# Optimization experiments

Measured on AMD Instinct MI355X. Metric: run time of the kernel, lower is better.

Reference implementation:

```python
import jax, jax.numpy as jnp
import numpy as np

B, S, L, H, N_ITEMS = 16, 20, 64, 768, 50000  # sessions, max items/session, tokens/item, hidden, catalog
T = S * L
TEMP = 0.05       # config.temp
PAD_POS = 50      # pad item position id (see torch code)
EPS = 1e-8        # torch CosineSimilarity eps


def setup_inputs() -> dict:
    key = jax.random.key(0)
    k1, k2, k3, k4 = jax.random.split(key, 4)
    hidden = jax.random.normal(k1, (B, T, H), jnp.float32)
    emb = jax.random.normal(k2, (N_ITEMS, H), jnp.float32)
    # item position ids: each item's L tokens share position 1..S; padded items -> 50
    pos = np.tile(np.repeat(np.arange(1, S + 1), L)[None, :], (B, 1))  # [B,T]
    sess_len = np.asarray(jax.random.randint(k3, (B,), S // 2, S + 1))  # items per session
    item_idx = np.repeat(np.arange(S), L)[None, :]                      # [1,T]
    pos = np.where(item_idx < sess_len[:, None], pos, PAD_POS).astype(np.int32)
    attn = (pos != PAD_POS).astype(np.int32)
    attrs = np.asarray(jax.random.randint(k4, (B, T), 0, 4)).astype(np.int32)
    return {
        "hidden_states": hidden,
        "item_embedding": emb,
        "attention_mask": jnp.asarray(attn),
        "item_position_ids": jnp.asarray(pos),
        "attr_type_ids": jnp.asarray(attrs),
    }


def reference(hidden_states, item_embedding, attention_mask, item_position_ids, attr_type_ids):
    # --- RecformerPooler (pooler_type='item'): nan-mean pool tokens per item ---
    item_ids = jnp.arange(1, S + 1, dtype=item_position_ids.dtype)
    mask = item_position_ids[:, None, :] == item_ids[None, :, None]      # [B,S,T]
    counts = mask.sum(-1)                                                # [B,S]
    valid = counts > 0                                                   # items present in session
    maskf = mask.astype(hidden_states.dtype)
    pooled = jnp.einsum('bst,bth->bsh', maskf, hidden_states)
    pooled = pooled / jnp.maximum(counts, 1)[..., None].astype(hidden_states.dtype)
    # (torch produces NaN rows for invalid items; we carry `valid` instead)

    # --- Similarity: cosine / temp vs full item catalog ---
    pn = jnp.maximum(jnp.linalg.norm(pooled, axis=-1, keepdims=True), EPS)
    en = jnp.maximum(jnp.linalg.norm(item_embedding, axis=-1, keepdims=True), EPS)
    sim = jnp.einsum('bsh,nh->bns', pooled / pn, item_embedding / en) / TEMP  # [B,N,S]

    # --- reduce_session('maxsim'): NaN -> -inf, max over session items ---
    sim = jnp.where(valid[:, None, :], sim, -jnp.inf)
    scores = sim.max(axis=-1)  # [B, N]; trailing mean over attr dim (size 1) is identity
    return scores
```

## Files before the change

kernel.cpp:

```cpp
#include <hip/hip_runtime.h>

#define B_ 16
#define S_ 20
#define L_ 64
#define T_ 1280
#define H_ 768
#define NITEMS 50000
#define TEMP 0.05f
#define EPSN 1e-8f

#define BM 80
#define BN 128
#define BK 32
#define NKT (H_ / BK)

typedef __attribute__((ext_vector_type(8))) short short8;
typedef __attribute__((ext_vector_type(4))) short short4v;
typedef __attribute__((ext_vector_type(4))) float f32x4;

__device__ __forceinline__ unsigned short f2bf(float f) {
    unsigned int u = __float_as_uint(f);
    u = u + 0x7FFFu + ((u >> 16) & 1u);
    return (unsigned short)(u >> 16);
}

__global__ __launch_bounds__(256) void pool_kernel(const float* __restrict__ hidden,
                                                   const int* __restrict__ pos,
                                                   unsigned short* __restrict__ A,
                                                   int* __restrict__ valid) {
    const int row = blockIdx.x;
    const int b = row / S_, s = row % S_;
    const int tid = threadIdx.x;
    const float* hbase = hidden + ((size_t)b * T_ + (size_t)s * L_) * H_;
    const int* pbase = pos + b * T_ + s * L_;

    float sum0 = 0.f, sum1 = 0.f, sum2 = 0.f;
    int cnt = 0;
#pragma unroll 4
    for (int t = 0; t < L_; ++t) {
        if (pbase[t] == s + 1) {
            const float* hp = hbase + (size_t)t * H_;
            sum0 += hp[tid];
            sum1 += hp[tid + 256];
            sum2 += hp[tid + 512];
            ++cnt;
        }
    }
    const float inv = 1.0f / (float)(cnt > 0 ? cnt : 1);
    const float a0 = sum0 * inv, a1 = sum1 * inv, a2 = sum2 * inv;

    float ss = a0 * a0 + a1 * a1 + a2 * a2;
#pragma unroll
    for (int off = 32; off; off >>= 1) ss += __shfl_xor(ss, off, 64);
    __shared__ float red[4];
    const int wave = tid >> 6, lane = tid & 63;
    if (lane == 0) red[wave] = ss;
    __syncthreads();
    const float tot = red[0] + red[1] + red[2] + red[3];
    const float pn = fmaxf(sqrtf(tot), EPSN);
    const float scale = 1.0f / (pn * TEMP);

    unsigned short* outp = A + (size_t)row * H_;
    outp[tid]       = f2bf(a0 * scale);
    outp[tid + 256] = f2bf(a1 * scale);
    outp[tid + 512] = f2bf(a2 * scale);
    if (tid == 0) valid[row] = (cnt > 0) ? 1 : 0;
}

__global__ __launch_bounds__(256) void gemm_kernel(const float* __restrict__ emb,
                                                   const unsigned short* __restrict__ A,
                                                   const int* __restrict__ valid,
                                                   float* __restrict__ out) {
    const int ntile = blockIdx.x;
    const int mtile = blockIdx.y;
    const int n0 = ntile * BN, m0 = mtile * BM;
    const int tid = threadIdx.x;
    const int wave = tid >> 6, lane = tid & 63, quad = lane >> 4, lq = lane & 15;

    __shared__ alignas(16) short As[BM * BK];
    __shared__ alignas(16) short Bs[BN * BK];
    __shared__ float sEn[BN];
    __shared__ int sValid[BM];

    if (tid < BM) sValid[tid] = valid[m0 + tid];

    const int rB = tid >> 1;
    const int cB = (tid & 1) * 16;
    const bool bOK = (n0 + rB) < NITEMS;
    const float* gB = emb + (size_t)(n0 + rB) * H_ + cB;

    const int aRow = tid >> 2, aCol = (tid & 3) * 8;
    const unsigned short* gA0 = A + (size_t)(m0 + aRow) * H_ + aCol;
    const unsigned short* gA1 = gA0 + (size_t)64 * H_;

    float rowSq = 0.f;
    f32x4 acc[5][2];
#pragma unroll
    for (int i = 0; i < 5; ++i)
#pragma unroll
        for (int j = 0; j < 2; ++j) acc[i][j] = (f32x4)0.f;

    for (int kt = 0; kt < NKT; ++kt) {
        const int k0 = kt * BK;
        float4 bv[4];
        if (bOK) {
            const float4* p = reinterpret_cast<const float4*>(gB + k0);
#pragma unroll
            for (int i = 0; i < 4; ++i) bv[i] = p[i];
        } else {
#pragma unroll
            for (int i = 0; i < 4; ++i) bv[i] = make_float4(0.f, 0.f, 0.f, 0.f);
        }
        uint4 av0 = *reinterpret_cast<const uint4*>(gA0 + k0);
        uint4 av1 = make_uint4(0, 0, 0, 0);
        if (tid < 64) av1 = *reinterpret_cast<const uint4*>(gA1 + k0);

        __syncthreads();

#pragma unroll
        for (int i = 0; i < 4; ++i)
            rowSq += bv[i].x * bv[i].x + bv[i].y * bv[i].y + bv[i].z * bv[i].z + bv[i].w * bv[i].w;

#pragma unroll
        for (int i = 0; i < 4; ++i) {
            short4v w;
            w[0] = (short)f2bf(bv[i].x);
            w[1] = (short)f2bf(bv[i].y);
            w[2] = (short)f2bf(bv[i].z);
            w[3] = (short)f2bf(bv[i].w);
            *reinterpret_cast<short4v*>(&Bs[rB * BK + cB + i * 4]) = w;
        }
        reinterpret_cast<uint4*>(As)[tid] = av0;
        if (tid < 64) reinterpret_cast<uint4*>(As)[256 + tid] = av1;

        __syncthreads();

        short8 aF[5], bF[2];
#pragma unroll
        for (int mf = 0; mf < 5; ++mf)
            aF[mf] = *reinterpret_cast<const short8*>(&As[(mf * 16 + lq) * BK + quad * 8]);
#pragma unroll
        for (int nf = 0; nf < 2; ++nf)
            bF[nf] = *reinterpret_cast<const short8*>(&Bs[(wave * 32 + nf * 16 + lq) * BK + quad * 8]);
#pragma unroll
        for (int mf = 0; mf < 5; ++mf)
#pragma unroll
            for (int nf = 0; nf < 2; ++nf)
                acc[mf][nf] = __builtin_amdgcn_mfma_f32_16x16x32_bf16(aF[mf], bF[nf], acc[mf][nf], 0, 0, 0);
    }

    rowSq += __shfl_xor(rowSq, 1, 64);
    if ((tid & 1) == 0) sEn[rB] = fmaxf(sqrtf(rowSq), EPSN);
    __syncthreads();

#pragma unroll
    for (int nf = 0; nf < 2; ++nf) {
        const int ncol = wave * 32 + nf * 16 + lq;
        const int n = n0 + ncol;
        const float en = sEn[ncol];
#pragma unroll
        for (int bb = 0; bb < 4; ++bb) {
            float lm = -__builtin_inff();
#pragma unroll
            for (int mf = 0; mf < 5; ++mf)
#pragma unroll
                for (int e = 0; e < 4; ++e) {
                    const int r = mf * 16 + quad * 4 + e;
                    if (r >= bb * 20 && r < bb * 20 + 20 && sValid[r])
                        lm = fmaxf(lm, acc[mf][nf][e]);
                }
            lm = fmaxf(lm, __shfl_xor(lm, 16, 64));
            lm = fmaxf(lm, __shfl_xor(lm, 32, 64));
            if (quad == 0 && n < NITEMS)
                out[(size_t)(mtile * 4 + bb) * NITEMS + n] = lm / en;
        }
    }
}

extern "C" void kernel_launch(void* const* d_in, const int* in_sizes, int n_in,
                              void* d_out, int out_size, void* d_ws, size_t ws_size,
                              hipStream_t stream) {
    const float* hidden = (const float*)d_in[0];
    const float* emb    = (const float*)d_in[1];
    const int*   pos    = (const int*)d_in[3];
    float* out = (float*)d_out;

    unsigned short* Abf = (unsigned short*)d_ws;
    int* valid = (int*)((char*)d_ws + (size_t)320 * 768 * 2);

    pool_kernel<<<dim3(320), dim3(256), 0, stream>>>(hidden, pos, Abf, valid);
    gemm_kernel<<<dim3(391, 4), dim3(256), 0, stream>>>(emb, Abf, valid, out);
}
```

Measured before the change: 346.5 us.

## Cover all 320 session rows per GEMM block and double-buffer via global_load_lds

```diff
diff --git a/kernel.cpp b/kernel.cpp
--- a/kernel.cpp
+++ b/kernel.cpp
@@ -9,7 +9,7 @@
 #define TEMP 0.05f
 #define EPSN 1e-8f
 
-#define BM 80
+#define BM 320
 #define BN 128
 #define BK 32
 #define NKT (H_ / BK)
@@ -24,155 +24,185 @@
     return (unsigned short)(u >> 16);
 }
 
-__global__ __launch_bounds__(256) void pool_kernel(const float* __restrict__ hidden,
+typedef __attribute__((address_space(3))) void lds_void;
+typedef const __attribute__((address_space(1))) void gbl_void;
+__device__ __forceinline__ void load_lds16(const void* g, void* l) {
+    __builtin_amdgcn_global_load_lds((gbl_void*)g, (lds_void*)l, 16, 0, 0);
+}
+
+__global__ __launch_bounds__(192) void pool_kernel(const float* __restrict__ hidden,
                                                    const int* __restrict__ pos,
                                                    unsigned short* __restrict__ A,
                                                    int* __restrict__ valid) {
     const int row = blockIdx.x;
     const int b = row / S_, s = row % S_;
     const int tid = threadIdx.x;
-    const float* hbase = hidden + ((size_t)b * T_ + (size_t)s * L_) * H_;
+
+    __shared__ float wgt[L_];
+    __shared__ int cntS;
+    __shared__ float red[3];
+
     const int* pbase = pos + b * T_ + s * L_;
-
-    float sum0 = 0.f, sum1 = 0.f, sum2 = 0.f;
-    int cnt = 0;
-#pragma unroll 4
+    if (tid < L_) {
+        const int match = (pbase[tid] == s + 1) ? 1 : 0;
+        unsigned long long bal = __ballot(match);
+        wgt[tid] = match ? 1.0f : 0.0f;
+        if (tid == 0) cntS = (int)__popcll(bal);
+    }
+    __syncthreads();
+
+    const int cnt = cntS;
+    const float inv = 1.0f / (float)(cnt > 0 ? cnt : 1);
+    const float* hbase = hidden + ((size_t)b * T_ + (size_t)s * L_) * H_ + tid * 4;
+
+    float a0 = 0.f, a1 = 0.f, a2 = 0.f, a3 = 0.f;
+#pragma unroll 8
     for (int t = 0; t < L_; ++t) {
-        if (pbase[t] == s + 1) {
-            const float* hp = hbase + (size_t)t * H_;
-            sum0 += hp[tid];
-            sum1 += hp[tid + 256];
-            sum2 += hp[tid + 512];
-            ++cnt;
-        }
-    }
-    const float inv = 1.0f / (float)(cnt > 0 ? cnt : 1);
-    const float a0 = sum0 * inv, a1 = sum1 * inv, a2 = sum2 * inv;
-
-    float ss = a0 * a0 + a1 * a1 + a2 * a2;
+        const float w = wgt[t];
+        const float4 v = *reinterpret_cast<const float4*>(hbase + (size_t)t * H_);
+        a0 += w * v.x; a1 += w * v.y; a2 += w * v.z; a3 += w * v.w;
+    }
+    a0 *= inv; a1 *= inv; a2 *= inv; a3 *= inv;
+
+    float ss = a0 * a0 + a1 * a1 + a2 * a2 + a3 * a3;
 #pragma unroll
     for (int off = 32; off; off >>= 1) ss += __shfl_xor(ss, off, 64);
-    __shared__ float red[4];
     const int wave = tid >> 6, lane = tid & 63;
     if (lane == 0) red[wave] = ss;
     __syncthreads();
-    const float tot = red[0] + red[1] + red[2] + red[3];
-    const float pn = fmaxf(sqrtf(tot), EPSN);
-    const float scale = 1.0f / (pn * TEMP);
-
-    unsigned short* outp = A + (size_t)row * H_;
-    outp[tid]       = f2bf(a0 * scale);
-    outp[tid + 256] = f2bf(a1 * scale);
-    outp[tid + 512] = f2bf(a2 * scale);
+    const float tot = red[0] + red[1] + red[2];
+    const float scale = 1.0f / (fmaxf(sqrtf(tot), EPSN) * TEMP);
+
+    short4v w4;
+    w4[0] = (short)f2bf(a0 * scale);
+    w4[1] = (short)f2bf(a1 * scale);
+    w4[2] = (short)f2bf(a2 * scale);
+    w4[3] = (short)f2bf(a3 * scale);
+    *reinterpret_cast<short4v*>(A + (size_t)row * H_ + tid * 4) = w4;
     if (tid == 0) valid[row] = (cnt > 0) ? 1 : 0;
 }
 
-__global__ __launch_bounds__(256) void gemm_kernel(const float* __restrict__ emb,
-                                                   const unsigned short* __restrict__ A,
-                                                   const int* __restrict__ valid,
-                                                   float* __restrict__ out) {
-    const int ntile = blockIdx.x;
-    const int mtile = blockIdx.y;
-    const int n0 = ntile * BN, m0 = mtile * BM;
+__global__ __launch_bounds__(256, 2) void gemm_kernel(const float* __restrict__ emb,
+                                                      const unsigned short* __restrict__ A,
+                                                      const int* __restrict__ valid,
+                                                      float* __restrict__ out) {
+    const int n0 = blockIdx.x * BN;
     const int tid = threadIdx.x;
     const int wave = tid >> 6, lane = tid & 63, quad = lane >> 4, lq = lane & 15;
 
-    __shared__ alignas(16) short As[BM * BK];
-    __shared__ alignas(16) short Bs[BN * BK];
+    __shared__ alignas(16) short As[2][BM * BK];
+    __shared__ alignas(16) float Bs[2][BN * BK];
     __shared__ float sEn[BN];
-    __shared__ int sValid[BM];
-
-    if (tid < BM) sValid[tid] = valid[m0 + tid];
-
-    const int rB = tid >> 1;
-    const int cB = (tid & 1) * 16;
-    const bool bOK = (n0 + rB) < NITEMS;
-    const float* gB = emb + (size_t)(n0 + rB) * H_ + cB;
-
-    const int aRow = tid >> 2, aCol = (tid & 3) * 8;
-    const unsigned short* gA0 = A + (size_t)(m0 + aRow) * H_ + aCol;
-    const unsigned short* gA1 = gA0 + (size_t)64 * H_;
+    __shared__ int sMask[B_];
+
+    if (tid < B_) {
+        int m = 0;
+        for (int s = 0; s < S_; ++s) m |= (valid[tid * S_ + s] ? 1 : 0) << s;
+        sMask[tid] = m;
+    }
+
+    const unsigned short* aSrc = A + (size_t)(tid >> 2) * H_ + (tid & 3) * 8;
+    const float* bSrc[4];
+#pragma unroll
+    for (int i = 0; i < 4; ++i) {
+        int r = n0 + (tid >> 3) + i * 32;
+        if (r > NITEMS - 1) r = NITEMS - 1;
+        bSrc[i] = emb + (size_t)r * H_ + (tid & 7) * 4;
+    }
+
+#pragma unroll
+    for (int i = 0; i < 5; ++i)
+        load_lds16(aSrc + i * 64 * H_, (char*)(&As[0][0]) + tid * 16 + i * 4096);
+#pragma unroll
+    for (int i = 0; i < 4; ++i)
+        load_lds16(bSrc[i], (char*)(&Bs[0][0]) + tid * 16 + i * 4096);
 
     float rowSq = 0.f;
-    f32x4 acc[5][2];
-#pragma unroll
-    for (int i = 0; i < 5; ++i)
-#pragma unroll
-        for (int j = 0; j < 2; ++j) acc[i][j] = (f32x4)0.f;
-
+    f32x4 acc[20][2];
+#pragma unroll
+    for (int i = 0; i < 20; ++i) {
+        acc[i][0] = (f32x4)0.f;
+        acc[i][1] = (f32x4)0.f;
+    }
+
+    int cur = 0;
     for (int kt = 0; kt < NKT; ++kt) {
-        const int k0 = kt * BK;
-        float4 bv[4];
-        if (bOK) {
-            const float4* p = reinterpret_cast<const float4*>(gB + k0);
-#pragma unroll
-            for (int i = 0; i < 4; ++i) bv[i] = p[i];
-        } else {
-#pragma unroll
-            for (int i = 0; i < 4; ++i) bv[i] = make_float4(0.f, 0.f, 0.f, 0.f);
-        }
-        uint4 av0 = *reinterpret_cast<const uint4*>(gA0 + k0);
-        uint4 av1 = make_uint4(0, 0, 0, 0);
-        if (tid < 64) av1 = *reinterpret_cast<const uint4*>(gA1 + k0);
-
         __syncthreads();
-
-#pragma unroll
-        for (int i = 0; i < 4; ++i)
-            rowSq += bv[i].x * bv[i].x + bv[i].y * bv[i].y + bv[i].z * bv[i].z + bv[i].w * bv[i].w;
-
-#pragma unroll
-        for (int i = 0; i < 4; ++i) {
-            short4v w;
-            w[0] = (short)f2bf(bv[i].x);
-            w[1] = (short)f2bf(bv[i].y);
-            w[2] = (short)f2bf(bv[i].z);
-            w[3] = (short)f2bf(bv[i].w);
-            *reinterpret_cast<short4v*>(&Bs[rB * BK + cB + i * 4]) = w;
-        }
-        reinterpret_cast<uint4*>(As)[tid] = av0;
-        if (tid < 64) reinterpret_cast<uint4*>(As)[256 + tid] = av1;
-
-        __syncthreads();
-
-        short8 aF[5], bF[2];
-#pragma unroll
-        for (int mf = 0; mf < 5; ++mf)
-            aF[mf] = *reinterpret_cast<const short8*>(&As[(mf * 16 + lq) * BK + quad * 8]);
-#pragma unroll
-        for (int nf = 0; nf < 2; ++nf)
-            bF[nf] = *reinterpret_cast<const short8*>(&Bs[(wave * 32 + nf * 16 + lq) * BK + quad * 8]);
-#pragma unroll
-        for (int mf = 0; mf < 5; ++mf)
-#pragma unroll
-            for (int nf = 0; nf < 2; ++nf)
-                acc[mf][nf] = __builtin_amdgcn_mfma_f32_16x16x32_bf16(aF[mf], bF[nf], acc[mf][nf], 0, 0, 0);
+        if (kt + 1 < NKT) {
+            const int k0 = (kt + 1) * BK;
+#pragma unroll
+            for (int i = 0; i < 5; ++i)
+                load_lds16(aSrc + k0 + i * 64 * H_,
+                           (char*)(&As[cur ^ 1][0]) + tid * 16 + i * 4096);
+#pragma unroll
+            for (int i = 0; i < 4; ++i)
+                load_lds16(bSrc[i] + k0,
+                           (char*)(&Bs[cur ^ 1][0]) + tid * 16 + i * 4096);
+        }
+
+        {
+            const float* ep = &Bs[cur][(tid >> 1) * BK + (tid & 1) * 16];
+#pragma unroll
+            for (int i = 0; i < 4; ++i) {
+                const float4 v = *reinterpret_cast<const float4*>(ep + i * 4);
+                rowSq += v.x * v.x + v.y * v.y + v.z * v.z + v.w * v.w;
+            }
+        }
+
+        short8 bF[2];
+#pragma unroll
+        for (int nf = 0; nf < 2; ++nf) {
+            const float* bp = &Bs[cur][(wave * 32 + nf * 16 + lq) * BK + quad * 8];
+            const float4 x = *reinterpret_cast<const float4*>(bp);
+            const float4 y = *reinterpret_cast<const float4*>(bp + 4);
+            short8 f;
+            f[0] = (short)f2bf(x.x); f[1] = (short)f2bf(x.y);
+            f[2] = (short)f2bf(x.z); f[3] = (short)f2bf(x.w);
+            f[4] = (short)f2bf(y.x); f[5] = (short)f2bf(y.y);
+            f[6] = (short)f2bf(y.z); f[7] = (short)f2bf(y.w);
+            bF[nf] = f;
+        }
+
+#pragma unroll
+        for (int mf = 0; mf < 20; ++mf) {
+            const short8 aF =
+                *reinterpret_cast<const short8*>(&As[cur][(mf * 16 + lq) * BK + quad * 8]);
+            acc[mf][0] = __builtin_amdgcn_mfma_f32_16x16x32_bf16(aF, bF[0], acc[mf][0], 0, 0, 0);
+            acc[mf][1] = __builtin_amdgcn_mfma_f32_16x16x32_bf16(aF, bF[1], acc[mf][1], 0, 0, 0);
+        }
+        cur ^= 1;
     }
 
     rowSq += __shfl_xor(rowSq, 1, 64);
-    if ((tid & 1) == 0) sEn[rB] = fmaxf(sqrtf(rowSq), EPSN);
+    if (!(tid & 1)) sEn[tid >> 1] = fmaxf(sqrtf(rowSq), EPSN);
     __syncthreads();
 
 #pragma unroll
     for (int nf = 0; nf < 2; ++nf) {
         const int ncol = wave * 32 + nf * 16 + lq;
         const int n = n0 + ncol;
-        const float en = sEn[ncol];
-#pragma unroll
-        for (int bb = 0; bb < 4; ++bb) {
+        if (n >= NITEMS) continue;
+        const float inv_en = 1.0f / sEn[ncol];
+#pragma unroll
+        for (int bb = 0; bb < B_; ++bb) {
+            const int rLo = bb * S_;
+            const int msk = sMask[bb];
             float lm = -__builtin_inff();
-#pragma unroll
-            for (int mf = 0; mf < 5; ++mf)
+            const int mfLo = rLo >> 4;
+            const int mfHi = (rLo + S_ - 1) >> 4;
+#pragma unroll
+            for (int mf = mfLo; mf <= mfHi; ++mf)
 #pragma unroll
                 for (int e = 0; e < 4; ++e) {
                     const int r = mf * 16 + quad * 4 + e;
-                    if (r >= bb * 20 && r < bb * 20 + 20 && sValid[r])
-                        lm = fmaxf(lm, acc[mf][nf][e]);
+                    const unsigned off = (unsigned)(r - rLo);
+                    const bool ok = (off < (unsigned)S_) && ((msk >> off) & 1);
+                    lm = ok ? fmaxf(lm, acc[mf][nf][e]) : lm;
                 }
             lm = fmaxf(lm, __shfl_xor(lm, 16, 64));
             lm = fmaxf(lm, __shfl_xor(lm, 32, 64));
-            if (quad == 0 && n < NITEMS)
-                out[(size_t)(mtile * 4 + bb) * NITEMS + n] = lm / en;
+            if (quad == 0)
+                out[(size_t)bb * NITEMS + n] = lm * inv_en;
         }
     }
 }
@@ -188,6 +218,6 @@
     unsigned short* Abf = (unsigned short*)d_ws;
     int* valid = (int*)((char*)d_ws + (size_t)320 * 768 * 2);
 
-    pool_kernel<<<dim3(320), dim3(256), 0, stream>>>(hidden, pos, Abf, valid);
-    gemm_kernel<<<dim3(391, 4), dim3(256), 0, stream>>>(emb, Abf, valid, out);
-}
+    pool_kernel<<<dim3(320), dim3(192), 0, stream>>>(hidden, pos, Abf, valid);
+    gemm_kernel<<<dim3((NITEMS + BN - 1) / BN), dim3(256), 0, stream>>>(emb, Abf, valid, out);
+}
```

Result: faster. 299.0 us (-13.7%).
